# Kernel optimization log

Measured on AMD Instinct MI355X. Metric: run time of the kernel, lower is better.

Reference implementation:

```python
import jax, jax.numpy as jnp
import numpy as np

N_NODES = 50000
N_EDGES = 800000
N_HIDDEN = 64
N_LAYER = 3
IN_DIM = 4


def setup_inputs() -> dict:
    key = jax.random.key(0)
    ks = jax.random.split(key, 10)
    x = jax.random.normal(ks[0], (N_NODES, IN_DIM), dtype=jnp.float32)
    edge_index = jax.random.randint(ks[1], (2, N_EDGES), 0, N_NODES, dtype=jnp.int64)
    # Glorot-style params matching pyg GCNConv (lin has no bias; conv adds bias after aggregation)
    def glorot(k, fan_in, fan_out):
        s = jnp.sqrt(6.0 / (fan_in + fan_out))
        return jax.random.uniform(k, (fan_in, fan_out), jnp.float32, -s, s)
    W_in = glorot(ks[2], IN_DIM, N_HIDDEN)
    b_in = jnp.zeros((N_HIDDEN,), jnp.float32)
    W_h = jnp.stack([glorot(jax.random.fold_in(ks[3], i), N_HIDDEN, N_HIDDEN) for i in range(N_LAYER)])
    b_h = jnp.zeros((N_LAYER, N_HIDDEN), jnp.float32)
    W_out = glorot(ks[4], N_HIDDEN, 1)
    b_out = jnp.zeros((1,), jnp.float32)
    return {"x": x, "edge_index": edge_index, "W_in": W_in, "b_in": b_in,
            "W_h": W_h, "b_h": b_h, "W_out": W_out, "b_out": b_out}


def _gcn_norm(edge_index, n_nodes):
    # add self-loops, compute symmetric norm D^{-1/2} (A+I) D^{-1/2}
    loop = jnp.arange(n_nodes, dtype=edge_index.dtype)
    src = jnp.concatenate([edge_index[0], loop])
    dst = jnp.concatenate([edge_index[1], loop])
    deg = jax.ops.segment_sum(jnp.ones_like(dst, dtype=jnp.float32), dst, num_segments=n_nodes)
    dinv = jax.lax.rsqrt(deg)  # deg >= 1 due to self-loops
    norm = dinv[src] * dinv[dst]
    return src, dst, norm


def _gcn_conv(x, W, b, src, dst, norm, n_nodes):
    h = x @ W                                   # [N, out]
    msg = h[src] * norm[:, None]                # gather + scale, [E+N, out]
    out = jax.ops.segment_sum(msg, dst, num_segments=n_nodes)  # scatter-add
    return out + b


def reference(x, edge_index, W_in, b_in, W_h, b_h, W_out, b_out):
    n = x.shape[0]
    src, dst, norm = _gcn_norm(edge_index, n)
    h = jax.nn.relu(_gcn_conv(x, W_in, b_in, src, dst, norm, n))
    for i in range(W_h.shape[0]):
        h = jax.nn.relu(_gcn_conv(h, W_h[i], b_h[i], src, dst, norm, n))
    return _gcn_conv(h, W_out, b_out, src, dst, norm, n)
```

## Files before the change

kernel.cpp:

```cpp
#include <hip/hip_runtime.h>
#include <hip/hip_bf16.h>


#define TPB 256
#define EPT 8
#define CHUNK (TPB * EPT)
typedef __hip_bfloat16 bf16;
#define B2F __bfloat162float

__global__ void k_zero_b(int* __restrict__ bktcnt, int* __restrict__ ticket) {
    bktcnt[threadIdx.x] = 0;
    if (threadIdx.x == 0) *ticket = 0;
}

__global__ __launch_bounds__(TPB) void k_bktcnt(
    const int* __restrict__ dst, int* __restrict__ bktcnt, int* __restrict__ ticket,
    int* __restrict__ bktbase, int* __restrict__ bcur, int E, int n) {
    __shared__ int h[256];
    __shared__ int lastFlag;
    int tid = threadIdx.x;
    h[tid] = 0;
    __syncthreads();
    int e0 = blockIdx.x * CHUNK;
#pragma unroll
    for (int u = 0; u < EPT; ++u) {
        int e = e0 + u * TPB + tid;
        if (e < E) {
            int d = dst[e];
            if ((unsigned)d < (unsigned)n) atomicAdd(&h[d >> 8], 1);
        }
    }
    __syncthreads();
    if (h[tid]) atomicAdd(&bktcnt[tid], h[tid]);
    __threadfence();
    __syncthreads();
    if (tid == 0) lastFlag = (atomicAdd(ticket, 1) == (int)gridDim.x - 1);
    __syncthreads();
    if (!lastFlag) return;
    int v = atomicAdd(&bktcnt[tid], 0);
    h[tid] = v;
    __syncthreads();
    for (int off = 1; off < 256; off <<= 1) {
        int u2 = (tid >= off) ? h[tid - off] : 0;
        __syncthreads();
        h[tid] += u2;
        __syncthreads();
    }
    int excl = h[tid] - v;
    bktbase[tid] = excl;
    bcur[tid] = excl;
    if (tid == 255) bktbase[256] = h[tid];
}

__global__ __launch_bounds__(TPB) void k_bin(
    const int* __restrict__ src, const int* __restrict__ dst,
    int* __restrict__ bcur, unsigned* __restrict__ staging, int E, int n) {
    __shared__ int hcnt[256];
    __shared__ int hbase[256];
    int tid = threadIdx.x;
    int e0 = blockIdx.x * CHUNK;
    hcnt[tid] = 0;
    __syncthreads();

    int eb[EPT];
    unsigned rec[EPT];
#pragma unroll
    for (int u = 0; u < EPT; ++u) {
        int e = e0 + u * TPB + tid;
        eb[u] = -1;
        if (e < E) {
            int d = dst[e], s = src[e];
            if ((unsigned)d < (unsigned)n && (unsigned)s < (unsigned)n) {
                eb[u] = d >> 8;
                rec[u] = (unsigned)s | ((unsigned)(d & 255) << 16);
                atomicAdd(&hcnt[eb[u]], 1);
            }
        }
    }
    __syncthreads();
    int c = hcnt[tid];
    hbase[tid] = (c > 0) ? atomicAdd(&bcur[tid], c) : 0;
    hcnt[tid] = 0;
    __syncthreads();
#pragma unroll
    for (int u = 0; u < EPT; ++u) {
        if (eb[u] >= 0) {
            int r = atomicAdd(&hcnt[eb[u]], 1);
            int pos = hbase[eb[u]] + r;
            if ((unsigned)pos < (unsigned)E) staging[pos] = rec[u];
        }
    }
}

__global__ __launch_bounds__(TPB) void k_unbin2(
    const unsigned* __restrict__ staging, const int* __restrict__ bktbase,
    int* __restrict__ row_start, float* __restrict__ dinv,
    unsigned short* __restrict__ bucket, int E, int n) {
    __shared__ int cnt[256];
    __shared__ int scn[256];
    __shared__ int cur[256];
    int b = blockIdx.x, tid = threadIdx.x;
    int lo = bktbase[b], hi = bktbase[b + 1];
    lo = max(0, min(lo, E)); hi = max(lo, min(hi, E));

    cnt[tid] = 0;
    __syncthreads();
    for (int i = lo + tid; i < hi; i += TPB)
        atomicAdd(&cnt[(staging[i] >> 16) & 255], 1);
    __syncthreads();

    int v = cnt[tid];
    scn[tid] = v;
    __syncthreads();
    for (int off = 1; off < 256; off <<= 1) {
        int u = (tid >= off) ? scn[tid - off] : 0;
        __syncthreads();
        scn[tid] += u;
        __syncthreads();
    }
    int excl = scn[tid] - v;
    int base = min(lo + excl, E);
    cur[tid] = base;
    int d = (b << 8) + tid;
    if (d < n) {
        row_start[d] = base;
        dinv[d] = rsqrtf((float)v + 1.0f);
        if (d == n - 1) row_start[n] = min(base + v, E);
    }
    __syncthreads();

    for (int i = lo + tid; i < hi; i += TPB) {
        unsigned r = staging[i];
        int t = (r >> 16) & 255;
        int pos = atomicAdd(&cur[t], 1);
        if ((unsigned)pos < (unsigned)E) bucket[pos] = (unsigned short)(r & 0xffffu);
    }
}

__global__ void k_mm_in(const float* __restrict__ x, const float* __restrict__ W,
                        const float* __restrict__ dinv, bf16* __restrict__ g, int n) {
    int t = blockIdx.x * blockDim.x + threadIdx.x;
    if (t >= n * 64) return;
    int i = t >> 6, j = t & 63;
    float acc = 0.f;
#pragma unroll
    for (int k = 0; k < 4; ++k) acc = fmaf(x[i * 4 + k], W[k * 64 + j], acc);
    g[t] = __float2bfloat16(acc * dinv[i]);
}

__device__ __forceinline__ void acc_oct(float* a, uint4 w) {
    a[0] += __uint_as_float(w.x << 16);
    a[1] += __uint_as_float(w.x & 0xffff0000u);
    a[2] += __uint_as_float(w.y << 16);
    a[3] += __uint_as_float(w.y & 0xffff0000u);
    a[4] += __uint_as_float(w.z << 16);
    a[5] += __uint_as_float(w.z & 0xffff0000u);
    a[6] += __uint_as_float(w.w << 16);
    a[7] += __uint_as_float(w.w & 0xffff0000u);
}

__device__ __forceinline__ void agg_oct(const bf16* __restrict__ g,
                                        const unsigned short* __restrict__ bucket,
                                        int k0, int k1, int d, float* __restrict__ a,
                                        int lane, unsigned nm1, unsigned Em1) {
    int grp = lane >> 3, i = lane & 7;
#pragma unroll
    for (int m = 0; m < 8; ++m) a[m] = 0.f;
    if (grp == 0) {
        uint4 w = *(const uint4*)(g + (size_t)d * 64 + 8 * i);
        acc_oct(a, w);
    }
    for (int base = k0; base < k1; base += 64) {
        int cnt = min(64, k1 - base);
        int rec = bucket[min((unsigned)(base + lane), Em1)];
        int k = 0;
        for (; k + 16 <= cnt; k += 16) {
            unsigned s0 = min((unsigned)__shfl(rec, k + grp), nm1);
            unsigned s1 = min((unsigned)__shfl(rec, k + 8 + grp), nm1);
            uint4 w0 = *(const uint4*)(g + (size_t)s0 * 64 + 8 * i);
            uint4 w1 = *(const uint4*)(g + (size_t)s1 * 64 + 8 * i);
            acc_oct(a, w0);
            acc_oct(a, w1);
        }
        for (; k < cnt; k += 8) {
            int e = k + grp;
            unsigned s = min((unsigned)__shfl(rec, min(e, 63)), nm1);
            uint4 w = *(const uint4*)(g + (size_t)s * 64 + 8 * i);
            if (e < cnt) acc_oct(a, w);
        }
    }
}

__global__ __launch_bounds__(TPB, 4) void k_gconv(
    const bf16* __restrict__ gIn, const float* __restrict__ dinv,
    const int* __restrict__ row_start, const unsigned short* __restrict__ bucket,
    const float* __restrict__ bias, const float* __restrict__ W,
    bf16* __restrict__ gOut, int n, int E) {
    __shared__ float sVp[4][8][68];
    int tid = threadIdx.x;
    int r = tid >> 6, j = tid & 63;
    int grp = j >> 3, i = j & 7;
    unsigned nm1 = (unsigned)(n - 1), Em1 = (unsigned)(E - 1);

    float wreg[64];
#pragma unroll
    for (int k = 0; k < 64; ++k) wreg[k] = W[k * 64 + j];
    float bj = bias[j];

    int nw = gridDim.x * 4;
    for (int d = blockIdx.x * 4 + r; d < n; d += nw) {
        float dd = dinv[d];
        int k0 = row_start[d], k1 = row_start[d + 1];
        k1 = min(k1, E); k0 = max(min(k0, k1), 0);

        float a[8];
        agg_oct(gIn, bucket, k0, k1, d, a, j, nm1, Em1);

        float4* prow = (float4*)&sVp[r][grp][8 * i];
        prow[0] = make_float4(a[0], a[1], a[2], a[3]);
        prow[1] = make_float4(a[4], a[5], a[6], a[7]);
        float full = 0.f;
#pragma unroll
        for (int g = 0; g < 8; ++g) full += sVp[r][g][j];

        float act = fmaxf(fmaf(dd, full, bj), 0.f);
        sVp[r][0][j] = act;

        float acc0 = 0.f, acc1 = 0.f, acc2 = 0.f, acc3 = 0.f;
#pragma unroll
        for (int k4 = 0; k4 < 16; ++k4) {
            float4 av = *(const float4*)&sVp[r][0][4 * k4];
            acc0 = fmaf(av.x, wreg[4 * k4 + 0], acc0);
            acc1 = fmaf(av.y, wreg[4 * k4 + 1], acc1);
            acc2 = fmaf(av.z, wreg[4 * k4 + 2], acc2);
            acc3 = fmaf(av.w, wreg[4 * k4 + 3], acc3);
        }
        float acc = (acc0 + acc1) + (acc2 + acc3);
        gOut[(size_t)d * 64 + j] = __float2bfloat16(acc * dd);
    }
}

__global__ __launch_bounds__(TPB) void k_gconv_z(
    const bf16* __restrict__ gIn, const float* __restrict__ dinv,
    const int* __restrict__ row_start, const unsigned short* __restrict__ bucket,
    const float* __restrict__ bias, const float* __restrict__ Wout,
    float* __restrict__ zg, int n, int E) {
    __shared__ float sVp[4][8][68];
    int tid = threadIdx.x;
    int r = tid >> 6, j = tid & 63;
    int grp = j >> 3, i = j & 7;
    int d = blockIdx.x * 4 + r;
    if (d >= n) return;
    float dd = dinv[d];
    int k0 = row_start[d], k1 = row_start[d + 1];
    k1 = min(k1, E); k0 = max(min(k0, k1), 0);

    float a[8];
    agg_oct(gIn, bucket, k0, k1, d, a, j, (unsigned)(n - 1), (unsigned)(E - 1));

    float4* prow = (float4*)&sVp[r][grp][8 * i];
    prow[0] = make_float4(a[0], a[1], a[2], a[3]);
    prow[1] = make_float4(a[4], a[5], a[6], a[7]);
    float full = 0.f;
#pragma unroll
    for (int g = 0; g < 8; ++g) full += sVp[r][g][j];

    float p = fmaxf(fmaf(dd, full, bias[j]), 0.f) * Wout[j];
#pragma unroll
    for (int off = 32; off > 0; off >>= 1) p += __shfl_down(p, off);
    if (j == 0) zg[d] = p * dd;
}

__global__ __launch_bounds__(TPB) void k_out(
    const float* __restrict__ zg, const float* __restrict__ dinv,
    const int* __restrict__ row_start, const unsigned short* __restrict__ bucket,
    const float* __restrict__ b_out, float* __restrict__ out, int n, int E) {
    int t = blockIdx.x * blockDim.x + threadIdx.x;
    int d = t >> 6, lane = t & 63;
    if (d >= n) return;
    int k0 = row_start[d], k1 = row_start[d + 1];
    k1 = min(k1, E); k0 = max(min(k0, k1), 0);
    unsigned nm1 = (unsigned)(n - 1);
    float v = 0.f;
    for (int k = k0 + lane; k < k1; k += 64) {
        unsigned s = min((unsigned)bucket[k], nm1);
        v += zg[s];
    }
#pragma unroll
    for (int off = 32; off > 0; off >>= 1) v += __shfl_down(v, off);
    if (lane == 0) out[d] = fmaf(zg[d] + v, dinv[d], b_out[0]);
}

extern "C" void kernel_launch(void* const* d_in, const int* in_sizes, int n_in,
                              void* d_out, int out_size, void* d_ws, size_t ws_size,
                              hipStream_t stream) {
    const float* x     = (const float*)d_in[0];
    const int*   ei    = (const int*)d_in[1];
    const float* W_in  = (const float*)d_in[2];
    const float* b_in  = (const float*)d_in[3];
    const float* W_h   = (const float*)d_in[4];
    const float* b_h   = (const float*)d_in[5];
    const float* W_out = (const float*)d_in[6];
    const float* b_out = (const float*)d_in[7];
    float* out = (float*)d_out;

    int N = in_sizes[0] / 4;
    int E = in_sizes[1] / 2;
    const int* src = ei;
    const int* dst = ei + E;

    char* ws = (char*)d_ws;
    bf16* gA               = (bf16*)ws;           ws += (size_t)N * 64 * 2;
    bf16* gB               = (bf16*)ws;           ws += (size_t)N * 64 * 2;
    unsigned short* bucket = (unsigned short*)ws; ws += (size_t)E * 2;
    unsigned* staging      = (unsigned*)ws;       ws += (size_t)E * 4;
    int*  row_start        = (int*)ws;            ws += (size_t)(N + 1) * 4;
    float* dinv            = (float*)ws;          ws += (size_t)N * 4;
    float* zg              = (float*)ws;          ws += (size_t)N * 4;
    int*  bktcnt           = (int*)ws;            ws += 256 * 4;
    int*  ticket           = (int*)ws;            ws += 4;
    int*  bktbase          = (int*)ws;            ws += 257 * 4;
    int*  bcur             = (int*)ws;

    int B     = (N + 255) >> 8;
    int gNF   = (N * 64 + TPB - 1) / TPB;
    int gN4   = (N + 3) / 4;
    int gPers = 1024;
    int gBin  = (E + CHUNK - 1) / CHUNK;

    k_zero_b<<<1, 256, 0, stream>>>(bktcnt, ticket);
    k_bktcnt<<<gBin, TPB, 0, stream>>>(dst, bktcnt, ticket, bktbase, bcur, E, N);
    k_bin<<<gBin, TPB, 0, stream>>>(src, dst, bcur, staging, E, N);
    k_unbin2<<<B, TPB, 0, stream>>>(staging, bktbase, row_start, dinv, bucket, E, N);

    k_mm_in<<<gNF, TPB, 0, stream>>>(x, W_in, dinv, gA, N);
    k_gconv<<<gPers, TPB, 0, stream>>>(gA, dinv, row_start, bucket, b_in, W_h, gB, N, E);
    k_gconv<<<gPers, TPB, 0, stream>>>(gB, dinv, row_start, bucket, b_h, W_h + 4096, gA, N, E);
    k_gconv<<<gPers, TPB, 0, stream>>>(gA, dinv, row_start, bucket, b_h + 64, W_h + 8192, gB, N, E);
    k_gconv_z<<<gN4, TPB, 0, stream>>>(gB, dinv, row_start, bucket, b_h + 128, W_out, zg, N, E);
    k_out<<<gN4, TPB, 0, stream>>>(zg, dinv, row_start, bucket, b_out, out, N, E);
}
```

Before: 270.7 us.

## Aggregate 4-dim input features before the input projection in the first layer

Rather than projecting x to 64 dims and then aggregating bf16 rows, the first layer now aggregates the dinv-scaled 4-wide fp32 inputs, which are prepared in the unbin kernel. It then applies W_in, bias and ReLU, followed by the first hidden matmul, all inside a new fused kernel. This removes the k_mm_in launch and cuts per-edge gather traffic from 128 bytes to 16. The cost is a full wave reduction of four floats per node, plus a LDS write-read between the reduction and the matmul, which has no barrier between the sAct store and the loads.

```diff
diff --git a/kernel.cpp b/kernel.cpp
--- a/kernel.cpp
+++ b/kernel.cpp
@@ -94,6 +94,7 @@
 
 __global__ __launch_bounds__(TPB) void k_unbin2(
     const unsigned* __restrict__ staging, const int* __restrict__ bktbase,
+    const float* __restrict__ x, float4* __restrict__ xt,
     int* __restrict__ row_start, float* __restrict__ dinv,
     unsigned short* __restrict__ bucket, int E, int n) {
     __shared__ int cnt[256];
@@ -124,7 +125,11 @@
     int d = (b << 8) + tid;
     if (d < n) {
         row_start[d] = base;
-        dinv[d] = rsqrtf((float)v + 1.0f);
+        float di = rsqrtf((float)v + 1.0f);
+        dinv[d] = di;
+        float4 xv = ((const float4*)x)[d];
+        xv.x *= di; xv.y *= di; xv.z *= di; xv.w *= di;
+        xt[d] = xv;
         if (d == n - 1) row_start[n] = min(base + v, E);
     }
     __syncthreads();
@@ -135,17 +140,6 @@
         int pos = atomicAdd(&cur[t], 1);
         if ((unsigned)pos < (unsigned)E) bucket[pos] = (unsigned short)(r & 0xffffu);
     }
-}
-
-__global__ void k_mm_in(const float* __restrict__ x, const float* __restrict__ W,
-                        const float* __restrict__ dinv, bf16* __restrict__ g, int n) {
-    int t = blockIdx.x * blockDim.x + threadIdx.x;
-    if (t >= n * 64) return;
-    int i = t >> 6, j = t & 63;
-    float acc = 0.f;
-#pragma unroll
-    for (int k = 0; k < 4; ++k) acc = fmaf(x[i * 4 + k], W[k * 64 + j], acc);
-    g[t] = __float2bfloat16(acc * dinv[i]);
 }
 
 __device__ __forceinline__ void acc_oct(float* a, uint4 w) {
@@ -188,6 +182,62 @@
             uint4 w = *(const uint4*)(g + (size_t)s * 64 + 8 * i);
             if (e < cnt) acc_oct(a, w);
         }
+    }
+}
+
+__global__ __launch_bounds__(TPB, 4) void k_gconv1(
+    const float4* __restrict__ xt, const float* __restrict__ dinv,
+    const int* __restrict__ row_start, const unsigned short* __restrict__ bucket,
+    const float* __restrict__ W_in, const float* __restrict__ b_in,
+    const float* __restrict__ Wh0, bf16* __restrict__ gOut, int n, int E) {
+    __shared__ float sAct[4][64];
+    int tid = threadIdx.x;
+    int r = tid >> 6, j = tid & 63;
+    unsigned nm1 = (unsigned)(n - 1);
+
+    float wreg[64];
+#pragma unroll
+    for (int k = 0; k < 64; ++k) wreg[k] = Wh0[k * 64 + j];
+    float win0 = W_in[0 * 64 + j], win1 = W_in[1 * 64 + j];
+    float win2 = W_in[2 * 64 + j], win3 = W_in[3 * 64 + j];
+    float bj = b_in[j];
+
+    int nw = gridDim.x * 4;
+    for (int d = blockIdx.x * 4 + r; d < n; d += nw) {
+        float dd = dinv[d];
+        int k0 = row_start[d], k1 = row_start[d + 1];
+        k1 = min(k1, E); k0 = max(min(k0, k1), 0);
+
+        float4 v = make_float4(0.f, 0.f, 0.f, 0.f);
+        if (j == 0) v = xt[d];
+        for (int k = k0 + j; k < k1; k += 64) {
+            unsigned s = min((unsigned)bucket[k], nm1);
+            float4 t = xt[s];
+            v.x += t.x; v.y += t.y; v.z += t.z; v.w += t.w;
+        }
+#pragma unroll
+        for (int off = 1; off < 64; off <<= 1) {
+            v.x += __shfl_xor(v.x, off);
+            v.y += __shfl_xor(v.y, off);
+            v.z += __shfl_xor(v.z, off);
+            v.w += __shfl_xor(v.w, off);
+        }
+        float dot = fmaf(v.x, win0, fmaf(v.y, win1, fmaf(v.z, win2, v.w * win3)));
+        float act = fmaxf(fmaf(dd, dot, bj), 0.f);
+        sAct[r][j] = act;
+
+        float acc0 = 0.f, acc1 = 0.f, acc2 = 0.f, acc3 = 0.f;
+        const float4* ap = (const float4*)&sAct[r][0];
+#pragma unroll
+        for (int k4 = 0; k4 < 16; ++k4) {
+            float4 av = ap[k4];
+            acc0 = fmaf(av.x, wreg[4 * k4 + 0], acc0);
+            acc1 = fmaf(av.y, wreg[4 * k4 + 1], acc1);
+            acc2 = fmaf(av.z, wreg[4 * k4 + 2], acc2);
+            acc3 = fmaf(av.w, wreg[4 * k4 + 3], acc3);
+        }
+        float acc = (acc0 + acc1) + (acc2 + acc3);
+        gOut[(size_t)d * 64 + j] = __float2bfloat16(acc * dd);
     }
 }
 
@@ -312,6 +362,7 @@
     char* ws = (char*)d_ws;
     bf16* gA               = (bf16*)ws;           ws += (size_t)N * 64 * 2;
     bf16* gB               = (bf16*)ws;           ws += (size_t)N * 64 * 2;
+    float4* xt             = (float4*)ws;         ws += (size_t)N * 16;
     unsigned short* bucket = (unsigned short*)ws; ws += (size_t)E * 2;
     unsigned* staging      = (unsigned*)ws;       ws += (size_t)E * 4;
     int*  row_start        = (int*)ws;            ws += (size_t)(N + 1) * 4;
@@ -323,7 +374,6 @@
     int*  bcur             = (int*)ws;
 
     int B     = (N + 255) >> 8;
-    int gNF   = (N * 64 + TPB - 1) / TPB;
     int gN4   = (N + 3) / 4;
     int gPers = 1024;
     int gBin  = (E + CHUNK - 1) / CHUNK;
@@ -331,10 +381,9 @@
     k_zero_b<<<1, 256, 0, stream>>>(bktcnt, ticket);
     k_bktcnt<<<gBin, TPB, 0, stream>>>(dst, bktcnt, ticket, bktbase, bcur, E, N);
     k_bin<<<gBin, TPB, 0, stream>>>(src, dst, bcur, staging, E, N);
-    k_unbin2<<<B, TPB, 0, stream>>>(staging, bktbase, row_start, dinv, bucket, E, N);
-
-    k_mm_in<<<gNF, TPB, 0, stream>>>(x, W_in, dinv, gA, N);
-    k_gconv<<<gPers, TPB, 0, stream>>>(gA, dinv, row_start, bucket, b_in, W_h, gB, N, E);
+    k_unbin2<<<B, TPB, 0, stream>>>(staging, bktbase, x, xt, row_start, dinv, bucket, E, N);
+
+    k_gconv1<<<gPers, TPB, 0, stream>>>(xt, dinv, row_start, bucket, W_in, b_in, W_h, gB, N, E);
     k_gconv<<<gPers, TPB, 0, stream>>>(gB, dinv, row_start, bucket, b_h, W_h + 4096, gA, N, E);
     k_gconv<<<gPers, TPB, 0, stream>>>(gA, dinv, row_start, bucket, b_h + 64, W_h + 8192, gB, N, E);
     k_gconv_z<<<gN4, TPB, 0, stream>>>(gB, dinv, row_start, bucket, b_h + 128, W_out, zg, N, E);
```

Result: faster. 260.0 us, median of 2 (-4.0%).
